# Kernel tuning notes

Measured on AMD Instinct MI355X. Metric: run time of the kernel, lower is better.

The kernel has to match this reference:

```python
import jax, jax.numpy as jnp
import numpy as np

HIDDEN = 4096
N_HEADS = 32
HEAD_DIM = HIDDEN // N_HEADS  # 128
ROPE_BASE = 10000.0
NEG_INF = -1e9  # stands in for torch.finfo(dtype).min in the additive mask


def rotate_half(x):
    x1 = x[..., : x.shape[-1] // 2]
    x2 = x[..., x.shape[-1] // 2 :]
    return jnp.concatenate((-x2, x1), axis=-1)


def rope_tables(seq_len, dtype=jnp.float32):
    # RotaryEmbedding: inv_freq = 1/base^(arange(0,dim,2)/dim); emb = cat(freqs, freqs)
    inv_freq = 1.0 / (ROPE_BASE ** (jnp.arange(0, HEAD_DIM, 2, dtype=jnp.float32) / HEAD_DIM))
    t = jnp.arange(seq_len, dtype=jnp.float32)
    freqs = jnp.einsum('s,d->sd', t, inv_freq)          # [S, HEAD_DIM/2]
    emb = jnp.concatenate((freqs, freqs), axis=-1)      # [S, HEAD_DIM]
    return jnp.cos(emb).astype(dtype), jnp.sin(emb).astype(dtype)


def setup_inputs() -> dict:
    key = jax.random.key(0)
    k0, k1, k2 = jax.random.split(key, 3)
    B, S = 1, 2048
    hidden_states = jax.random.normal(k0, (B, S, HIDDEN), dtype=jnp.float32)
    W_pack = jax.random.normal(k1, (3 * HIDDEN, HIDDEN), dtype=jnp.float32) * 0.02
    W_o = jax.random.normal(k2, (HIDDEN, HIDDEN), dtype=jnp.float32) * 0.02
    position_ids = jnp.broadcast_to(jnp.arange(S, dtype=jnp.int32)[None, :], (B, S))
    # additive causal mask [B, 1, S, S]
    causal = jnp.tril(jnp.ones((S, S), dtype=bool))
    attention_mask = jnp.where(causal, 0.0, NEG_INF).astype(jnp.float32)[None, None, :, :]
    attention_mask = jnp.broadcast_to(attention_mask, (B, 1, S, S))
    return {
        'hidden_states': hidden_states,
        'attention_mask': attention_mask,
        'position_ids': position_ids,
        'W_pack': W_pack,
        'W_o': W_o,
    }


def reference(hidden_states, attention_mask, position_ids, W_pack, W_o):
    B, S, H = hidden_states.shape
    norm_factor = 1.0 / np.sqrt(HEAD_DIM)

    # fused QKV projection: Linear(H, 3H, bias=False)
    proj = jnp.einsum('bsh,ph->bsp', hidden_states, W_pack)        # [B, S, 3H]
    q, k, v = jnp.split(proj, 3, axis=-1)

    def to_heads(x):
        return x.reshape(B, S, N_HEADS, HEAD_DIM).transpose(0, 2, 1, 3)  # [B, nH, S, D]

    q, k, v = to_heads(q), to_heads(k), to_heads(v)

    # RoPE (gather per position_ids, matching apply_rotary_pos_emb with unsqueeze_dim=1)
    cos_t, sin_t = rope_tables(S, hidden_states.dtype)
    cos = cos_t[position_ids][:, None, :, :]  # [B, 1, S, D]
    sin = sin_t[position_ids][:, None, :, :]
    q = q * cos + rotate_half(q) * sin
    k = k * cos + rotate_half(k) * sin

    # manual QK^T / softmax / AV (prefill: KV-cache update is a plain copy of cur)
    scores = jnp.einsum('bhqd,bhkd->bhqk', q, k) * norm_factor + attention_mask
    probs = jax.nn.softmax(scores, axis=-1)
    attn = jnp.einsum('bhqk,bhkd->bhqd', probs, v)                 # [B, nH, S, D]

    attn = attn.transpose(0, 2, 1, 3).reshape(B, S, H)
    return jnp.einsum('bsh,oh->bso', attn, W_o)
```

## Files before the change

### kernel.cpp

```cpp
#include <hip/hip_runtime.h>
#include <math.h>

typedef __bf16 bf16x8 __attribute__((ext_vector_type(8)));
typedef __bf16 bf16x4 __attribute__((ext_vector_type(4)));
typedef float f32x4 __attribute__((ext_vector_type(4)));

#define S_LEN 2048
#define NHEADS 32
#define DHEAD 128
#define HID 4096

__device__ __forceinline__ void gld16(const void* g, void* l) {
  __builtin_amdgcn_global_load_lds(
      (const __attribute__((address_space(1))) unsigned int*)g,
      (__attribute__((address_space(3))) unsigned int*)l, 16, 0, 0);
}

__global__ __launch_bounds__(256) void cvt_k(const float4* __restrict__ in,
                                             __bf16* __restrict__ out, int n4) {
  int i = blockIdx.x * 256 + threadIdx.x;
  if (i >= n4) return;
  float4 f = in[i];
  bf16x4 o;
  o[0] = (__bf16)f.x; o[1] = (__bf16)f.y; o[2] = (__bf16)f.z; o[3] = (__bf16)f.w;
  *(bf16x4*)(out + (size_t)i * 4) = o;
}

template <int ND, int KD, int EPI>
__global__ __launch_bounds__(256) void gemm_bt(const __bf16* __restrict__ A,
                                               const __bf16* __restrict__ B,
                                               float* __restrict__ C,
                                               __bf16* __restrict__ Qh,
                                               __bf16* __restrict__ Kh,
                                               __bf16* __restrict__ Vh) {
  const int bn = blockIdx.x, bm = blockIdx.y;
  const int t = threadIdx.x;
  const int w = t >> 6, l = t & 63, quad = l >> 4, l15 = l & 15;
  const int wr = w >> 1, wc = w & 1;

  __shared__ __align__(16) __bf16 As[128 * 32];
  __shared__ __align__(16) __bf16 Bs[128 * 32];

  const f32x4 zero4 = {0.f, 0.f, 0.f, 0.f};
  f32x4 acc[4][4];
#pragma unroll
  for (int i = 0; i < 4; ++i)
#pragma unroll
    for (int j = 0; j < 4; ++j) acc[i][j] = zero4;

  const __bf16* Ab = A + (size_t)bm * 128 * KD;
  const __bf16* Bb = B + (size_t)bn * 128 * KD;

  for (int k0 = 0; k0 < KD; k0 += 32) {
    __syncthreads();
#pragma unroll
    for (int j = 0; j < 2; ++j) {
      const int c = j * 256 + t;
      const int row = c >> 2, kc = c & 3;
      const int cb = j * 256 + w * 64;
      gld16(Ab + (size_t)row * KD + k0 + kc * 8, As + (size_t)cb * 8);
      gld16(Bb + (size_t)row * KD + k0 + kc * 8, Bs + (size_t)cb * 8);
    }
    __syncthreads();
    bf16x8 af[4], bf_[4];
#pragma unroll
    for (int mi = 0; mi < 4; ++mi)
      af[mi] = *(const bf16x8*)(As + (wr * 64 + mi * 16 + l15) * 32 + quad * 8);
#pragma unroll
    for (int ni = 0; ni < 4; ++ni)
      bf_[ni] = *(const bf16x8*)(Bs + (wc * 64 + ni * 16 + l15) * 32 + quad * 8);
#pragma unroll
    for (int mi = 0; mi < 4; ++mi)
#pragma unroll
      for (int ni = 0; ni < 4; ++ni)
        acc[mi][ni] = __builtin_amdgcn_mfma_f32_16x16x32_bf16(af[mi], bf_[ni], acc[mi][ni], 0, 0, 0);
  }

#pragma unroll
  for (int mi = 0; mi < 4; ++mi)
#pragma unroll
    for (int ni = 0; ni < 4; ++ni)
#pragma unroll
      for (int r = 0; r < 4; ++r) {
        const int row = bm * 128 + wr * 64 + mi * 16 + quad * 4 + r;
        const int col = bn * 128 + wc * 64 + ni * 16 + l15;
        const float v = acc[mi][ni][r];
        if constexpr (EPI == 0) {
          C[(size_t)row * ND + col] = v;
        } else {
          const int part = col >> 12;
          const int cl = col & 4095;
          const int hh = cl >> 7, d = cl & 127;
          __bf16* dst = (part == 0) ? Qh : (part == 1) ? Kh : Vh;
          dst[(size_t)(hh * S_LEN + row) * DHEAD + d] = (__bf16)v;
        }
      }
}

__global__ __launch_bounds__(256) void rope_k(__bf16* __restrict__ Q, __bf16* __restrict__ K) {
  const int idx = blockIdx.x * 256 + threadIdx.x;
  const int i = idx & 63;
  const int s = (idx >> 6) & (S_LEN - 1);
  const int h = idx >> 17;
  const float inv_freq = __expf(-9.210340371976184f * (float)i * (1.0f / 64.0f));
  float sn, cs;
  sincosf((float)s * inv_freq, &sn, &cs);
  const size_t base = (size_t)(h * S_LEN + s) * DHEAD;
  const float q0 = (float)Q[base + i], q1 = (float)Q[base + i + 64];
  Q[base + i]      = (__bf16)(q0 * cs - q1 * sn);
  Q[base + i + 64] = (__bf16)(q1 * cs + q0 * sn);
  const float k0 = (float)K[base + i], k1 = (float)K[base + i + 64];
  K[base + i]      = (__bf16)(k0 * cs - k1 * sn);
  K[base + i + 64] = (__bf16)(k1 * cs + k0 * sn);
}

__global__ __launch_bounds__(256) void vtrans_k(const __bf16* __restrict__ Vh,
                                                __bf16* __restrict__ Vt) {
  __shared__ __align__(16) __bf16 tile[64][72];
  const int s0 = blockIdx.x * 64, d0 = blockIdx.y * 64, h = blockIdx.z;
  const int t = threadIdx.x;
#pragma unroll
  for (int j = 0; j < 2; ++j) {
    const int idx = j * 256 + t;
    const int r = idx >> 3, c8 = idx & 7;
    const bf16x8 v = *(const bf16x8*)(Vh + (size_t)(h * S_LEN + s0 + r) * DHEAD + d0 + c8 * 8);
    *(bf16x8*)(&tile[r][c8 * 8]) = v;
  }
  __syncthreads();
#pragma unroll
  for (int j = 0; j < 2; ++j) {
    const int idx = j * 256 + t;
    const int rd = idx >> 3, c8 = idx & 7;
    bf16x8 v;
#pragma unroll
    for (int i = 0; i < 8; ++i) v[i] = tile[c8 * 8 + i][rd];
    *(bf16x8*)(Vt + (size_t)(h * DHEAD + d0 + rd) * S_LEN + s0 + c8 * 8) = v;
  }
}

__global__ __launch_bounds__(256) void flash_k(const __bf16* __restrict__ Qh,
                                               const __bf16* __restrict__ Kh,
                                               const __bf16* __restrict__ Vt,
                                               __bf16* __restrict__ ctx) {
  const int qt = (int)gridDim.x - 1 - (int)blockIdx.x;
  const int h = blockIdx.y;
  const int t = threadIdx.x;
  const int w = t >> 6, l = t & 63, quad = l >> 4, l15 = l & 15;

  __shared__ __align__(16) __bf16 Qs[64 * 128];
  __shared__ __align__(16) __bf16 Ks[64 * 128];
  __shared__ __align__(16) __bf16 Vts[128 * 64];
  __shared__ __align__(16) __bf16 Ps[4][16 * 72];

  const int q0 = qt * 64;

#pragma unroll
  for (int j = 0; j < 4; ++j) {
    const int c = j * 256 + t;
    const int row = c >> 4, dc = c & 15;
    const int cb = j * 256 + w * 64;
    gld16(Qh + (size_t)(h * S_LEN + q0 + row) * DHEAD + dc * 8, Qs + (size_t)cb * 8);
  }

  const f32x4 zero4 = {0.f, 0.f, 0.f, 0.f};
  float m_r[4], l_r[4];
  f32x4 o[8];
#pragma unroll
  for (int i = 0; i < 8; ++i) o[i] = zero4;
#pragma unroll
  for (int r = 0; r < 4; ++r) { m_r[r] = -INFINITY; l_r[r] = 0.f; }

  for (int kt = 0; kt <= qt; ++kt) {
    __syncthreads();
    const int k0 = kt * 64;
#pragma unroll
    for (int j = 0; j < 4; ++j) {
      const int c = j * 256 + t;
      const int cb = j * 256 + w * 64;
      const int row = c >> 4, dc = c & 15;
      gld16(Kh + (size_t)(h * S_LEN + k0 + row) * DHEAD + dc * 8, Ks + (size_t)cb * 8);
      const int d = c >> 3, kc = c & 7;
      gld16(Vt + (size_t)(h * DHEAD + d) * S_LEN + k0 + kc * 8, Vts + (size_t)cb * 8);
    }
    __syncthreads();

    f32x4 sacc[4];
#pragma unroll
    for (int ni = 0; ni < 4; ++ni) sacc[ni] = zero4;
#pragma unroll
    for (int ks = 0; ks < 4; ++ks) {
      const bf16x8 aq = *(const bf16x8*)(Qs + (w * 16 + l15) * 128 + ks * 32 + quad * 8);
#pragma unroll
      for (int ni = 0; ni < 4; ++ni) {
        const bf16x8 bk = *(const bf16x8*)(Ks + (ni * 16 + l15) * 128 + ks * 32 + quad * 8);
        sacc[ni] = __builtin_amdgcn_mfma_f32_16x16x32_bf16(aq, bk, sacc[ni], 0, 0, 0);
      }
    }

    const bool diag = (kt == qt);
#pragma unroll
    for (int ni = 0; ni < 4; ++ni)
#pragma unroll
      for (int r = 0; r < 4; ++r) {
        float v = sacc[ni][r] * 0.08838834764831845f;
        if (diag && (ni * 16 + l15 > w * 16 + quad * 4 + r)) v = -1e9f;
        sacc[ni][r] = v;
      }

    float mx[4];
#pragma unroll
    for (int r = 0; r < 4; ++r) {
      float v = fmaxf(fmaxf(sacc[0][r], sacc[1][r]), fmaxf(sacc[2][r], sacc[3][r]));
#pragma unroll
      for (int off = 1; off < 16; off <<= 1) v = fmaxf(v, __shfl_xor(v, off));
      mx[r] = v;
    }

    float alpha[4];
#pragma unroll
    for (int r = 0; r < 4; ++r) {
      const float mn = fmaxf(m_r[r], mx[r]);
      alpha[r] = __expf(m_r[r] - mn);
      m_r[r] = mn;
    }

    float rs[4] = {0.f, 0.f, 0.f, 0.f};
#pragma unroll
    for (int ni = 0; ni < 4; ++ni)
#pragma unroll
      for (int r = 0; r < 4; ++r) {
        const float p = __expf(sacc[ni][r] - m_r[r]);
        rs[r] += p;
        Ps[w][(quad * 4 + r) * 72 + ni * 16 + l15] = (__bf16)p;
      }
#pragma unroll
    for (int r = 0; r < 4; ++r) {
      float v = rs[r];
#pragma unroll
      for (int off = 1; off < 16; off <<= 1) v += __shfl_xor(v, off);
      l_r[r] = l_r[r] * alpha[r] + v;
    }

#pragma unroll
    for (int ni = 0; ni < 8; ++ni)
#pragma unroll
      for (int r = 0; r < 4; ++r) o[ni][r] = o[ni][r] * alpha[r];

#pragma unroll
    for (int ks = 0; ks < 2; ++ks) {
      const bf16x8 ap = *(const bf16x8*)(&Ps[w][l15 * 72 + ks * 32 + quad * 8]);
#pragma unroll
      for (int ni = 0; ni < 8; ++ni) {
        const bf16x8 bv = *(const bf16x8*)(Vts + (ni * 16 + l15) * 64 + ks * 32 + quad * 8);
        o[ni] = __builtin_amdgcn_mfma_f32_16x16x32_bf16(ap, bv, o[ni], 0, 0, 0);
      }
    }
  }

#pragma unroll
  for (int r = 0; r < 4; ++r) {
    const float inv = 1.f / l_r[r];
    const size_t qg = (size_t)q0 + w * 16 + quad * 4 + r;
#pragma unroll
    for (int ni = 0; ni < 8; ++ni)
      ctx[qg * HID + h * DHEAD + ni * 16 + l15] = (__bf16)(o[ni][r] * inv);
  }
}

extern "C" void kernel_launch(void* const* d_in, const int* in_sizes, int n_in,
                              void* d_out, int out_size, void* d_ws, size_t ws_size,
                              hipStream_t stream) {
  const float* hs = (const float*)d_in[0];
  const float* Wp = (const float*)d_in[3];
  const float* Wo = (const float*)d_in[4];
  float* out = (float*)d_out;

  char* p = (char*)d_ws;
  auto carve = [&](size_t elems) {
    __bf16* r = (__bf16*)p;
    p += ((elems * sizeof(__bf16) + 255) / 256) * 256;
    return r;
  };
  __bf16* Xb  = carve((size_t)S_LEN * HID);
  __bf16* Wpb = carve((size_t)3 * HID * HID);
  __bf16* Wob = carve((size_t)HID * HID);
  __bf16* Qh  = carve((size_t)S_LEN * HID);
  __bf16* Kh  = carve((size_t)S_LEN * HID);
  __bf16* Vh  = carve((size_t)S_LEN * HID);
  __bf16* Vt  = carve((size_t)S_LEN * HID);
  __bf16* ctx = carve((size_t)S_LEN * HID);

  cvt_k<<<(S_LEN * HID / 4) / 256, 256, 0, stream>>>((const float4*)hs, Xb, S_LEN * HID / 4);
  cvt_k<<<(3 * HID * HID / 4) / 256, 256, 0, stream>>>((const float4*)Wp, Wpb, 3 * HID * HID / 4);
  cvt_k<<<(HID * HID / 4) / 256, 256, 0, stream>>>((const float4*)Wo, Wob, HID * HID / 4);

  gemm_bt<3 * HID, HID, 1><<<dim3(96, 16), 256, 0, stream>>>(Xb, Wpb, nullptr, Qh, Kh, Vh);
  rope_k<<<(NHEADS * S_LEN * 64) / 256, 256, 0, stream>>>(Qh, Kh);
  vtrans_k<<<dim3(S_LEN / 64, DHEAD / 64, NHEADS), 256, 0, stream>>>(Vh, Vt);
  flash_k<<<dim3(S_LEN / 64, NHEADS), 256, 0, stream>>>(Qh, Kh, Vt, ctx);
  gemm_bt<HID, HID, 0><<<dim3(32, 16), 256, 0, stream>>>(ctx, Wob, out, nullptr, nullptr, nullptr);
}
```

Baseline: 1.025 ms.

## Swizzle LDS tiles to avoid bank conflicts and fold softmax scale into RoPE

Applies XOR/rotation-style swizzles to the shared-memory layouts of the GEMM A/B tiles and the attention Q, K and V^T tiles. The global-to-LDS chunk placement is permuted so that the MFMA operand reads from LDS spread across banks instead of conflicting. Separately, the 1/sqrt(d) scale is folded into the Q RoPE kernel, which removes the per-score multiply in the attention loop. This also changes bf16 rounding of Q slightly, and the swizzle index maths must match exactly between writes and reads.

Result: faster. 878.1 us (-14.3%).

```diff
diff --git a/kernel.cpp b/kernel.cpp
--- a/kernel.cpp
+++ b/kernel.cpp
@@ -56,19 +56,21 @@
 #pragma unroll
     for (int j = 0; j < 2; ++j) {
       const int c = j * 256 + t;
-      const int row = c >> 2, kc = c & 3;
+      const int row = c >> 2, kcs = c & 3;
+      const int kc = (kcs - (row >> 1)) & 3;
       const int cb = j * 256 + w * 64;
       gld16(Ab + (size_t)row * KD + k0 + kc * 8, As + (size_t)cb * 8);
       gld16(Bb + (size_t)row * KD + k0 + kc * 8, Bs + (size_t)cb * 8);
     }
     __syncthreads();
     bf16x8 af[4], bf_[4];
+    const int cq = (quad + (l15 >> 1)) & 3;
 #pragma unroll
     for (int mi = 0; mi < 4; ++mi)
-      af[mi] = *(const bf16x8*)(As + (wr * 64 + mi * 16 + l15) * 32 + quad * 8);
+      af[mi] = *(const bf16x8*)(As + (wr * 64 + mi * 16 + l15) * 32 + cq * 8);
 #pragma unroll
     for (int ni = 0; ni < 4; ++ni)
-      bf_[ni] = *(const bf16x8*)(Bs + (wc * 64 + ni * 16 + l15) * 32 + quad * 8);
+      bf_[ni] = *(const bf16x8*)(Bs + (wc * 64 + ni * 16 + l15) * 32 + cq * 8);
 #pragma unroll
     for (int mi = 0; mi < 4; ++mi)
 #pragma unroll
@@ -105,10 +107,11 @@
   const float inv_freq = __expf(-9.210340371976184f * (float)i * (1.0f / 64.0f));
   float sn, cs;
   sincosf((float)s * inv_freq, &sn, &cs);
+  const float nf = 0.08838834764831845f;
   const size_t base = (size_t)(h * S_LEN + s) * DHEAD;
   const float q0 = (float)Q[base + i], q1 = (float)Q[base + i + 64];
-  Q[base + i]      = (__bf16)(q0 * cs - q1 * sn);
-  Q[base + i + 64] = (__bf16)(q1 * cs + q0 * sn);
+  Q[base + i]      = (__bf16)((q0 * cs - q1 * sn) * nf);
+  Q[base + i + 64] = (__bf16)((q1 * cs + q0 * sn) * nf);
   const float k0 = (float)K[base + i], k1 = (float)K[base + i + 64];
   K[base + i]      = (__bf16)(k0 * cs - k1 * sn);
   K[base + i + 64] = (__bf16)(k1 * cs + k0 * sn);
@@ -157,7 +160,8 @@
 #pragma unroll
   for (int j = 0; j < 4; ++j) {
     const int c = j * 256 + t;
-    const int row = c >> 4, dc = c & 15;
+    const int row = c >> 4, dcs = c & 15;
+    const int dc = (dcs - row) & 15;
     const int cb = j * 256 + w * 64;
     gld16(Qh + (size_t)(h * S_LEN + q0 + row) * DHEAD + dc * 8, Qs + (size_t)cb * 8);
   }
@@ -177,9 +181,11 @@
     for (int j = 0; j < 4; ++j) {
       const int c = j * 256 + t;
       const int cb = j * 256 + w * 64;
-      const int row = c >> 4, dc = c & 15;
+      const int row = c >> 4, dcs = c & 15;
+      const int dc = (dcs - row) & 15;
       gld16(Kh + (size_t)(h * S_LEN + k0 + row) * DHEAD + dc * 8, Ks + (size_t)cb * 8);
-      const int d = c >> 3, kc = c & 7;
+      const int d = c >> 3, kcs = c & 7;
+      const int kc = (kcs - d) & 7;
       gld16(Vt + (size_t)(h * DHEAD + d) * S_LEN + k0 + kc * 8, Vts + (size_t)cb * 8);
     }
     __syncthreads();
@@ -189,23 +195,23 @@
     for (int ni = 0; ni < 4; ++ni) sacc[ni] = zero4;
 #pragma unroll
     for (int ks = 0; ks < 4; ++ks) {
-      const bf16x8 aq = *(const bf16x8*)(Qs + (w * 16 + l15) * 128 + ks * 32 + quad * 8);
+      const int cq = ((ks * 4 + quad + l15) & 15) * 8;
+      const bf16x8 aq = *(const bf16x8*)(Qs + (w * 16 + l15) * 128 + cq);
 #pragma unroll
       for (int ni = 0; ni < 4; ++ni) {
-        const bf16x8 bk = *(const bf16x8*)(Ks + (ni * 16 + l15) * 128 + ks * 32 + quad * 8);
+        const bf16x8 bk = *(const bf16x8*)(Ks + (ni * 16 + l15) * 128 + cq);
         sacc[ni] = __builtin_amdgcn_mfma_f32_16x16x32_bf16(aq, bk, sacc[ni], 0, 0, 0);
       }
     }
 
     const bool diag = (kt == qt);
-#pragma unroll
-    for (int ni = 0; ni < 4; ++ni)
-#pragma unroll
-      for (int r = 0; r < 4; ++r) {
-        float v = sacc[ni][r] * 0.08838834764831845f;
-        if (diag && (ni * 16 + l15 > w * 16 + quad * 4 + r)) v = -1e9f;
-        sacc[ni][r] = v;
-      }
+    if (diag) {
+#pragma unroll
+      for (int ni = 0; ni < 4; ++ni)
+#pragma unroll
+        for (int r = 0; r < 4; ++r)
+          if (ni * 16 + l15 > w * 16 + quad * 4 + r) sacc[ni][r] = -1e9f;
+    }
 
     float mx[4];
 #pragma unroll
@@ -251,7 +257,8 @@
       const bf16x8 ap = *(const bf16x8*)(&Ps[w][l15 * 72 + ks * 32 + quad * 8]);
 #pragma unroll
       for (int ni = 0; ni < 8; ++ni) {
-        const bf16x8 bv = *(const bf16x8*)(Vts + (ni * 16 + l15) * 64 + ks * 32 + quad * 8);
+        const int cv = ((ks * 4 + quad + l15) & 7) * 8;
+        const bf16x8 bv = *(const bf16x8*)(Vts + (ni * 16 + l15) * 64 + cv);
         o[ni] = __builtin_amdgcn_mfma_f32_16x16x32_bf16(ap, bv, o[ni], 0, 0, 0);
       }
     }
```
